# Performance work log

Hardware: AMD Instinct MI355X
Metric: run time of the kernel (lower is better)

Reference implementation:

```python
import jax, jax.numpy as jnp
import numpy as np

INDIM, OUTDIM, K, EXPAND = 256, 256, 3, 64
STRIDE, PAD, DIL, GROUPS = 1, 1, 1, 1


def _make_mask(rng):
    # expander connectivity: indim == outdim, so use the 'else' branch of the
    # torch code: for each input channel, pick EXPAND output channels.
    m = np.zeros((OUTDIM, INDIM), dtype=np.float32)
    for i in range(INDIM):
        x = rng.permutation(OUTDIM)[:EXPAND]
        m[x, i] = 1.0
    # repeat over the kernel spatial dims
    return np.broadcast_to(m[:, :, None, None], (OUTDIM, INDIM, K, K)).copy()


def setup_inputs() -> dict:
    key = jax.random.key(0)
    k1, k2 = jax.random.split(key)
    x = jax.random.normal(k1, (32, INDIM, 56, 56), dtype=jnp.float32)
    # kaiming_normal_(mode='fan_out'): std = sqrt(2 / (outdim * k * k))
    std = np.sqrt(2.0 / (OUTDIM * K * K)).astype(np.float32)
    weight = jax.random.normal(k2, (OUTDIM, INDIM, K, K), dtype=jnp.float32) * std
    mask = jnp.asarray(_make_mask(np.random.default_rng(0)))
    return {"x": x, "weight": weight, "mask": mask}


def reference(x, weight, mask) -> jnp.ndarray:
    w = weight * mask  # zero out non-expander connections
    return jax.lax.conv_general_dilated(
        x, w,
        window_strides=(STRIDE, STRIDE),
        padding=((PAD, PAD), (PAD, PAD)),
        rhs_dilation=(DIL, DIL),
        feature_group_count=GROUPS,
        dimension_numbers=("NCHW", "OIHW", "NCHW"),
    )
```

## Files before the change

kernel.cpp:

```cpp
#include <hip/hip_runtime.h>
#include <hip/hip_bf16.h>

typedef short short8 __attribute__((ext_vector_type(8)));
typedef float float4v __attribute__((ext_vector_type(4)));

#define NIMG 32
#define CIN 256
#define COUT 256
#define HH 56
#define WW 56
#define HP 58
#define WP 58
#define PIXIMG (HH * WW)
#define TOTPIX (NIMG * PIXIMG)
#define OUTSTRIDE_N (COUT * PIXIMG)
#define TR_BLOCKS (NIMG * HP * 4)

static constexpr size_t XT_ELEMS = (size_t)NIMG * HP * WP * CIN;
static constexpr size_t WT_ELEMS = (size_t)9 * COUT * CIN;

static __device__ __forceinline__ unsigned short f2bf(float f) {
    unsigned int u = __builtin_bit_cast(unsigned int, f);
    u = (u + 0x7fffu + ((u >> 16) & 1u)) >> 16;
    return (unsigned short)u;
}

static __device__ __forceinline__ void gl16(const unsigned short* g, char* l) {
    __builtin_amdgcn_global_load_lds(
        (const __attribute__((address_space(1))) void*)g,
        (__attribute__((address_space(3))) void*)l, 16, 0, 0);
}

__global__ __launch_bounds__(256) void k_pre(const float* __restrict__ x,
                                             const float* __restrict__ wgt,
                                             const float* __restrict__ msk,
                                             unsigned short* __restrict__ xt,
                                             unsigned short* __restrict__ wt) {
    int t = threadIdx.x;
    if (blockIdx.x >= TR_BLOCKS) {
        int g = (blockIdx.x - TR_BLOCKS) * 256 + t;
        const float* wp = wgt + (size_t)g * 9;
        const float* mp = msk + (size_t)g * 9;
#pragma unroll
        for (int tap = 0; tap < 9; ++tap)
            wt[(size_t)tap * (COUT * CIN) + g] = f2bf(wp[tap] * mp[tap]);
        return;
    }
    int b   = blockIdx.x;
    int icb = b & 3;
    int hp  = (b >> 2) % HP;
    int n   = b / (4 * HP);
    unsigned short* rowb = xt + ((size_t)(n * HP + hp) * WP) * CIN + icb * 64;

    if (hp == 0 || hp == HP - 1) {
        for (int idx = t; idx < WP * 8; idx += 256) {
            int wq = idx >> 3, q = idx & 7;
            *(uint4*)(rowb + (size_t)wq * CIN + q * 8) = (uint4){0, 0, 0, 0};
        }
        return;
    }
    int h = hp - 1;
    __shared__ __align__(16) char lds[64 * 128];
    int w = t & 63, icl0 = t >> 6;
    if (w < WW) {
        const float* src = x + ((size_t)(n * CIN + icb * 64 + icl0) * HH + h) * WW + w;
#pragma unroll
        for (int j = 0; j < 16; ++j) {
            float v = src[(size_t)(j * 4) * PIXIMG];
            int icl = icl0 + j * 4;
            *(unsigned short*)(lds + w * 128 + ((icl * 2) ^ ((w & 7) << 4))) = f2bf(v);
        }
    }
    __syncthreads();
    int ic4 = t & 15, wr = t >> 4;
    unsigned short* dst = rowb + (size_t)CIN + ic4 * 4;
#pragma unroll
    for (int p = 0; p < 4; ++p) {
        int w2 = wr + p * 16;
        if (w2 < WW) {
            uint2 v = *(const uint2*)(lds + w2 * 128 + ((ic4 * 8) ^ ((w2 & 7) << 4)));
            *(uint2*)(dst + (size_t)w2 * CIN) = v;
        }
    }
    if (t < 32) {
        int col = (t >> 4) * (WP - 1);
        *(uint2*)(rowb + (size_t)col * CIN + (t & 15) * 4) = (uint2){0, 0};
    }
}

__global__ __launch_bounds__(256, 4) void k_conv(const unsigned short* __restrict__ xt,
                                                 const unsigned short* __restrict__ wt,
                                                 float* __restrict__ out) {
    __shared__ __align__(16) char lds[64 * 132 * 4];

    const int t    = threadIdx.x;
    const int lane = t & 63;
    const int wid  = t >> 6;
    const int woc  = wid >> 1;
    const int wpx  = wid & 1;

    const int b0 = blockIdx.x;
    const int b  = (b0 & 7) * 196 + (b0 >> 3);
    const int ptile = b >> 1;
    const int ocb   = b & 1;

    const int rl  = lane >> 3;
    const int sc  = ((lane & 7) ^ rl) * 8;
    const unsigned short* aS[4];
    const unsigned short* bS[4];
    char* dA[4];
    char* dB[4];
#pragma unroll
    for (int c = 0; c < 4; ++c) {
        int r = wid * 32 + c * 8 + rl;
        aS[c] = wt + (size_t)(ocb * 128 + r) * CIN + sc;
        int pg  = ptile * 128 + r;
        int n   = pg / PIXIMG;
        int rem = pg - n * PIXIMG;
        int h   = rem / WW, w = rem - h * WW;
        bS[c] = xt + ((size_t)((n * HP + h) * WP + w)) * CIN + sc;
        dA[c] = lds + (wid * 32 + c * 8) * 128;
        dB[c] = lds + 16384 + (wid * 32 + c * 8) * 128;
    }

    const int l15  = lane & 15;
    const int lg   = lane >> 4;
    const int swzf = (lane & 7) << 4;
    int colk[2];
    colk[0] = (lg * 16) ^ swzf;
    colk[1] = (64 + lg * 16) ^ swzf;
    int rowA[4], rowB[4];
#pragma unroll
    for (int i = 0; i < 4; ++i) {
        rowA[i] = (woc * 64 + i * 16 + l15) * 128;
        rowB[i] = 16384 + (wpx * 64 + i * 16 + l15) * 128;
    }

    float4v acc[4][4];
#pragma unroll
    for (int i = 0; i < 4; ++i)
#pragma unroll
        for (int j = 0; j < 4; ++j)
            acc[i][j] = (float4v){0.f, 0.f, 0.f, 0.f};

#pragma unroll 1
    for (int s = 0; s < 36; ++s) {
        const int tap = s >> 2;
        const int dh  = (tap * 86) >> 8;
        const int dw  = tap - dh * 3;
        const size_t ao = (size_t)tap * (COUT * CIN) + (size_t)((s & 3) << 6);
        const size_t bo = (size_t)(dh * WP + dw) * CIN + (size_t)((s & 3) << 6);
#pragma unroll
        for (int c = 0; c < 4; ++c) gl16(aS[c] + ao, dA[c]);
#pragma unroll
        for (int c = 0; c < 4; ++c) gl16(bS[c] + bo, dB[c]);
        __syncthreads();
#pragma unroll
        for (int kk = 0; kk < 2; ++kk) {
            short8 af[4], bfr[4];
#pragma unroll
            for (int i = 0; i < 4; ++i)
                af[i] = *(const short8*)(lds + rowA[i] + colk[kk]);
#pragma unroll
            for (int i = 0; i < 4; ++i)
                bfr[i] = *(const short8*)(lds + rowB[i] + colk[kk]);
#pragma unroll
            for (int oi = 0; oi < 4; ++oi)
#pragma unroll
                for (int pi = 0; pi < 4; ++pi)
                    acc[oi][pi] = __builtin_amdgcn_mfma_f32_16x16x32_bf16(
                        af[oi], bfr[pi], acc[oi][pi], 0, 0, 0);
        }
        __syncthreads();
    }

    float* ep = (float*)lds;
#pragma unroll 1
    for (int c = 0; c < 2; ++c) {
        if (woc == c) {
#pragma unroll
            for (int oi = 0; oi < 4; ++oi)
#pragma unroll
                for (int pi = 0; pi < 4; ++pi)
#pragma unroll
                    for (int r = 0; r < 4; ++r)
                        ep[(oi * 16 + lg * 4 + r) * 132 +
                           (wpx * 64 + pi * 16 + l15)] = acc[oi][pi][r];
        }
        __syncthreads();
        const int rrow = t >> 5;
        const int rcol = (t & 31) * 4;
        int pg  = ptile * 128 + rcol;
        int n2  = pg / PIXIMG;
        int rem = pg - n2 * PIXIMG;
        float* ob = out + (size_t)n2 * OUTSTRIDE_N +
                    (size_t)(ocb * 128 + c * 64) * PIXIMG + rem;
#pragma unroll
        for (int rd = 0; rd < 8; ++rd) {
            int row = rd * 8 + rrow;
            float4v v = *(const float4v*)&ep[row * 132 + rcol];
            *(float4v*)(ob + (size_t)row * PIXIMG) = v;
        }
        __syncthreads();
    }
}

__global__ __launch_bounds__(256) void k_naive(const float* __restrict__ x,
                                               const float* __restrict__ wg,
                                               const float* __restrict__ mk,
                                               float* __restrict__ out, int total) {
    int idx = blockIdx.x * 256 + threadIdx.x;
    if (idx >= total) return;
    int w  = idx % WW;
    int h  = (idx / WW) % HH;
    int oc = (idx / PIXIMG) % COUT;
    int n  = idx / (COUT * PIXIMG);
    float s = 0.f;
    for (int ic = 0; ic < CIN; ++ic) {
        const float* xp = x + (size_t)(n * CIN + ic) * PIXIMG;
        const float* wp = wg + (size_t)(oc * CIN + ic) * 9;
        const float* mp = mk + (size_t)(oc * CIN + ic) * 9;
#pragma unroll
        for (int kh = 0; kh < 3; ++kh) {
            int hy = h + kh - 1;
            if ((unsigned)hy >= HH) continue;
#pragma unroll
            for (int kw = 0; kw < 3; ++kw) {
                int wx = w + kw - 1;
                if ((unsigned)wx >= WW) continue;
                s += xp[hy * WW + wx] * wp[kh * 3 + kw] * mp[kh * 3 + kw];
            }
        }
    }
    out[idx] = s;
}

extern "C" void kernel_launch(void* const* d_in, const int* in_sizes, int n_in,
                              void* d_out, int out_size, void* d_ws, size_t ws_size,
                              hipStream_t stream) {
    const float* x  = (const float*)d_in[0];
    const float* wg = (const float*)d_in[1];
    const float* mk = (const float*)d_in[2];
    float* out = (float*)d_out;

    size_t need = XT_ELEMS * 2 + WT_ELEMS * 2 + 256;
    if (ws_size < need) {
        int total = NIMG * COUT * PIXIMG;
        k_naive<<<(total + 255) / 256, 256, 0, stream>>>(x, wg, mk, out, total);
        return;
    }

    unsigned short* xt = (unsigned short*)d_ws;
    unsigned short* wt = (unsigned short*)((char*)d_ws + XT_ELEMS * 2);

    k_pre<<<TR_BLOCKS + (COUT * CIN) / 256, 256, 0, stream>>>(x, wg, mk, xt, wt);
    k_conv<<<(TOTPIX / 128) * 2, 256, 0, stream>>>(xt, wt, out);
}
```

Before: 151.4 us.

## Reuse a halo-extended input slab in LDS across all nine conv taps

The implicit-GEMM conv now tiles over padded pixel positions. Each block loads a 248-row input slab, covering its 128 pixels plus a one-row halo on each side, into LDS once per 64-channel block. All nine taps read from that slab at shifted row offsets, so the input is no longer reloaded for every tap. Output is written with per-element validity checks that drop padding positions, which wastes some compute and turns the epilogue into scalar stores. The larger LDS footprint lowers the occupancy target from 4 to 3 blocks per CU.

Result: slower. 155.8 us (+2.9%).

```diff
diff --git a/kernel.cpp b/kernel.cpp
--- a/kernel.cpp
+++ b/kernel.cpp
@@ -12,11 +12,13 @@
 #define HP 58
 #define WP 58
 #define PIXIMG (HH * WW)
-#define TOTPIX (NIMG * PIXIMG)
+#define QIMG (HP * WP)
+#define QTOT (NIMG * QIMG)
+#define NTILE (QTOT / 128)
 #define OUTSTRIDE_N (COUT * PIXIMG)
 #define TR_BLOCKS (NIMG * HP * 4)
 
-static constexpr size_t XT_ELEMS = (size_t)NIMG * HP * WP * CIN;
+static constexpr size_t XT_ELEMS = (size_t)QTOT * CIN;
 static constexpr size_t WT_ELEMS = (size_t)9 * COUT * CIN;
 
 static __device__ __forceinline__ unsigned short f2bf(float f) {
@@ -88,10 +90,10 @@
     }
 }
 
-__global__ __launch_bounds__(256, 4) void k_conv(const unsigned short* __restrict__ xt,
+__global__ __launch_bounds__(256, 3) void k_conv(const unsigned short* __restrict__ xt,
                                                  const unsigned short* __restrict__ wt,
                                                  float* __restrict__ out) {
-    __shared__ __align__(16) char lds[64 * 132 * 4];
+    __shared__ __align__(16) char lds[48128];
 
     const int t    = threadIdx.x;
     const int lane = t & 63;
@@ -99,28 +101,23 @@
     const int woc  = wid >> 1;
     const int wpx  = wid & 1;
 
-    const int b0 = blockIdx.x;
-    const int b  = (b0 & 7) * 196 + (b0 >> 3);
-    const int ptile = b >> 1;
-    const int ocb   = b & 1;
-
-    const int rl  = lane >> 3;
-    const int sc  = ((lane & 7) ^ rl) * 8;
+    const int xcd = blockIdx.x & 7;
+    const int idx = blockIdx.x >> 3;
+    const int wg  = (xcd < 2) ? xcd * 211 + idx : 422 + (xcd - 2) * 210 + idx;
+    const int ptile = wg >> 1;
+    const int ocb   = wg & 1;
+    const int q0    = ptile * 128;
+
+    const int rl = lane >> 3;
+    const int sc = ((lane & 7) ^ rl) * 8;
+
     const unsigned short* aS[4];
-    const unsigned short* bS[4];
     char* dA[4];
-    char* dB[4];
 #pragma unroll
     for (int c = 0; c < 4; ++c) {
         int r = wid * 32 + c * 8 + rl;
         aS[c] = wt + (size_t)(ocb * 128 + r) * CIN + sc;
-        int pg  = ptile * 128 + r;
-        int n   = pg / PIXIMG;
-        int rem = pg - n * PIXIMG;
-        int h   = rem / WW, w = rem - h * WW;
-        bS[c] = xt + ((size_t)((n * HP + h) * WP + w)) * CIN + sc;
         dA[c] = lds + (wid * 32 + c * 8) * 128;
-        dB[c] = lds + 16384 + (wid * 32 + c * 8) * 128;
     }
 
     const int l15  = lane & 15;
@@ -129,12 +126,10 @@
     int colk[2];
     colk[0] = (lg * 16) ^ swzf;
     colk[1] = (64 + lg * 16) ^ swzf;
-    int rowA[4], rowB[4];
-#pragma unroll
-    for (int i = 0; i < 4; ++i) {
+    int rowA[4];
+#pragma unroll
+    for (int i = 0; i < 4; ++i)
         rowA[i] = (woc * 64 + i * 16 + l15) * 128;
-        rowB[i] = 16384 + (wpx * 64 + i * 16 + l15) * 128;
-    }
 
     float4v acc[4][4];
 #pragma unroll
@@ -144,37 +139,62 @@
             acc[i][j] = (float4v){0.f, 0.f, 0.f, 0.f};
 
 #pragma unroll 1
-    for (int s = 0; s < 36; ++s) {
-        const int tap = s >> 2;
-        const int dh  = (tap * 86) >> 8;
-        const int dw  = tap - dh * 3;
-        const size_t ao = (size_t)tap * (COUT * CIN) + (size_t)((s & 3) << 6);
-        const size_t bo = (size_t)(dh * WP + dw) * CIN + (size_t)((s & 3) << 6);
-#pragma unroll
-        for (int c = 0; c < 4; ++c) gl16(aS[c] + ao, dA[c]);
-#pragma unroll
-        for (int c = 0; c < 4; ++c) gl16(bS[c] + bo, dB[c]);
-        __syncthreads();
-#pragma unroll
-        for (int kk = 0; kk < 2; ++kk) {
-            short8 af[4], bfr[4];
-#pragma unroll
-            for (int i = 0; i < 4; ++i)
-                af[i] = *(const short8*)(lds + rowA[i] + colk[kk]);
-#pragma unroll
-            for (int i = 0; i < 4; ++i)
-                bfr[i] = *(const short8*)(lds + rowB[i] + colk[kk]);
-#pragma unroll
-            for (int oi = 0; oi < 4; ++oi)
-#pragma unroll
-                for (int pi = 0; pi < 4; ++pi)
-                    acc[oi][pi] = __builtin_amdgcn_mfma_f32_16x16x32_bf16(
-                        af[oi], bfr[pi], acc[oi][pi], 0, 0, 0);
-        }
-        __syncthreads();
+    for (int icb = 0; icb < 4; ++icb) {
+        for (int k = wid; k < 31; k += 4) {
+            int qr = q0 - 59 + 8 * k;
+            qr = (qr < 0) ? 0 : ((qr > QTOT - 8) ? QTOT - 8 : qr);
+            gl16(xt + (size_t)(qr + rl) * CIN + icb * 64 + sc,
+                 lds + 16384 + k * 1024);
+        }
+#pragma unroll
+        for (int tap = 0; tap < 9; ++tap) {
+            const size_t ao = (size_t)tap * (COUT * CIN) + icb * 64;
+#pragma unroll
+            for (int c = 0; c < 4; ++c) gl16(aS[c] + ao, dA[c]);
+            __syncthreads();
+            const int dh    = (tap * 86) >> 8;
+            const int dw    = tap - dh * 3;
+            const int delta = (dh - 1) * WP + (dw - 1);
+            const int rbb   = 59 + delta + wpx * 64 + l15;
+#pragma unroll
+            for (int kk = 0; kk < 2; ++kk) {
+                short8 af[4], bf[4];
+#pragma unroll
+                for (int i = 0; i < 4; ++i)
+                    af[i] = *(const short8*)(lds + rowA[i] + colk[kk]);
+#pragma unroll
+                for (int i = 0; i < 4; ++i) {
+                    int rb = rbb + i * 16;
+                    bf[i] = *(const short8*)(lds + 16384 + rb * 128 +
+                                             ((kk * 64 + lg * 16) ^ ((rb & 7) << 4)));
+                }
+#pragma unroll
+                for (int oi = 0; oi < 4; ++oi)
+#pragma unroll
+                    for (int pi = 0; pi < 4; ++pi)
+                        acc[oi][pi] = __builtin_amdgcn_mfma_f32_16x16x32_bf16(
+                            af[oi], bf[pi], acc[oi][pi], 0, 0, 0);
+            }
+            __syncthreads();
+        }
     }
 
     float* ep = (float*)lds;
+    const int rcol = (t & 31) * 4;
+    bool vld[4];
+    float* obase[4];
+#pragma unroll
+    for (int cc = 0; cc < 4; ++cc) {
+        int q  = q0 + rcol + cc;
+        int n  = q / QIMG;
+        int r2 = q - n * QIMG;
+        int hp = r2 / WP;
+        int wp = r2 - hp * WP;
+        vld[cc] = ((unsigned)(hp - 1) < (unsigned)HH) &&
+                  ((unsigned)(wp - 1) < (unsigned)WW);
+        obase[cc] = out + (size_t)n * OUTSTRIDE_N +
+                    (size_t)(ocb * 128) * PIXIMG + (hp - 1) * WW + (wp - 1);
+    }
 #pragma unroll 1
     for (int c = 0; c < 2; ++c) {
         if (woc == c) {
@@ -189,17 +209,14 @@
         }
         __syncthreads();
         const int rrow = t >> 5;
-        const int rcol = (t & 31) * 4;
-        int pg  = ptile * 128 + rcol;
-        int n2  = pg / PIXIMG;
-        int rem = pg - n2 * PIXIMG;
-        float* ob = out + (size_t)n2 * OUTSTRIDE_N +
-                    (size_t)(ocb * 128 + c * 64) * PIXIMG + rem;
 #pragma unroll
         for (int rd = 0; rd < 8; ++rd) {
             int row = rd * 8 + rrow;
             float4v v = *(const float4v*)&ep[row * 132 + rcol];
-            *(float4v*)(ob + (size_t)row * PIXIMG) = v;
+            size_t ro = (size_t)(c * 64 + row) * PIXIMG;
+#pragma unroll
+            for (int cc = 0; cc < 4; ++cc)
+                if (vld[cc]) obase[cc][ro] = v[cc];
         }
         __syncthreads();
     }
@@ -254,5 +271,5 @@
     unsigned short* wt = (unsigned short*)((char*)d_ws + XT_ELEMS * 2);
 
     k_pre<<<TR_BLOCKS + (COUT * CIN) / 256, 256, 0, stream>>>(x, wg, mk, xt, wt);
-    k_conv<<<(TOTPIX / 128) * 2, 256, 0, stream>>>(xt, wt, out);
-}
+    k_conv<<<NTILE * 2, 256, 0, stream>>>(xt, wt, out);
+}
```

## Pre-swizzle weights into MFMA fragment layout and load A directly to registers

Applied to the files above, without the earlier changes.

The weight preprocessing now writes bf16 weights in a fragment-ordered layout, so each lane can load its MFMA A operand straight from global memory as a contiguous short8. The conv kernel no longer stages weights through LDS; only the input tile goes through LDS, which halves LDS traffic and the LDS reads per step. It also lowers the occupancy hint from 4 to 3 waves to leave room for the extra registers holding both k-halves of A. The cost is more global/L2 load traffic from every wave, with latency that is only partly hidden before the barrier.

Result: slower. 160.3 us (+5.9%).

```diff
diff --git a/kernel.cpp b/kernel.cpp
--- a/kernel.cpp
+++ b/kernel.cpp
@@ -35,15 +35,20 @@
                                              const float* __restrict__ wgt,
                                              const float* __restrict__ msk,
                                              unsigned short* __restrict__ xt,
-                                             unsigned short* __restrict__ wt) {
+                                             unsigned short* __restrict__ wtF) {
     int t = threadIdx.x;
     if (blockIdx.x >= TR_BLOCKS) {
-        int g = (blockIdx.x - TR_BLOCKS) * 256 + t;
+        int g  = (blockIdx.x - TR_BLOCKS) * 256 + t;
+        int oc = g >> 8;
+        int ic = g & 255;
+        int fbl = ((ic >> 6) << 3) + (((ic >> 5) & 1) << 2) + ((ic >> 3) & 3);
+        int j   = ic & 7;
         const float* wp = wgt + (size_t)g * 9;
         const float* mp = msk + (size_t)g * 9;
 #pragma unroll
         for (int tap = 0; tap < 9; ++tap)
-            wt[(size_t)tap * (COUT * CIN) + g] = f2bf(wp[tap] * mp[tap]);
+            wtF[(size_t)(tap * 32 + fbl) * 2048 + oc * 8 + j] =
+                f2bf(wp[tap] * mp[tap]);
         return;
     }
     int b   = blockIdx.x;
@@ -88,8 +93,8 @@
     }
 }
 
-__global__ __launch_bounds__(256, 4) void k_conv(const unsigned short* __restrict__ xt,
-                                                 const unsigned short* __restrict__ wt,
+__global__ __launch_bounds__(256, 3) void k_conv(const unsigned short* __restrict__ xt,
+                                                 const unsigned short* __restrict__ wtF,
                                                  float* __restrict__ out) {
     __shared__ __align__(16) char lds[64 * 132 * 4];
 
@@ -106,21 +111,17 @@
 
     const int rl  = lane >> 3;
     const int sc  = ((lane & 7) ^ rl) * 8;
-    const unsigned short* aS[4];
     const unsigned short* bS[4];
-    char* dA[4];
     char* dB[4];
 #pragma unroll
     for (int c = 0; c < 4; ++c) {
         int r = wid * 32 + c * 8 + rl;
-        aS[c] = wt + (size_t)(ocb * 128 + r) * CIN + sc;
         int pg  = ptile * 128 + r;
         int n   = pg / PIXIMG;
         int rem = pg - n * PIXIMG;
         int h   = rem / WW, w = rem - h * WW;
         bS[c] = xt + ((size_t)((n * HP + h) * WP + w)) * CIN + sc;
-        dA[c] = lds + (wid * 32 + c * 8) * 128;
-        dB[c] = lds + 16384 + (wid * 32 + c * 8) * 128;
+        dB[c] = lds + (wid * 32 + c * 8) * 128;
     }
 
     const int l15  = lane & 15;
@@ -129,12 +130,13 @@
     int colk[2];
     colk[0] = (lg * 16) ^ swzf;
     colk[1] = (64 + lg * 16) ^ swzf;
-    int rowA[4], rowB[4];
-#pragma unroll
-    for (int i = 0; i < 4; ++i) {
-        rowA[i] = (woc * 64 + i * 16 + l15) * 128;
-        rowB[i] = 16384 + (wpx * 64 + i * 16 + l15) * 128;
-    }
+    int rowB[4];
+#pragma unroll
+    for (int i = 0; i < 4; ++i)
+        rowB[i] = (wpx * 64 + i * 16 + l15) * 128;
+
+    const unsigned short* aBase =
+        wtF + (size_t)lg * 2048 + (size_t)(ocb * 128 + woc * 64 + l15) * 8;
 
     float4v acc[4][4];
 #pragma unroll
@@ -148,19 +150,22 @@
         const int tap = s >> 2;
         const int dh  = (tap * 86) >> 8;
         const int dw  = tap - dh * 3;
-        const size_t ao = (size_t)tap * (COUT * CIN) + (size_t)((s & 3) << 6);
         const size_t bo = (size_t)(dh * WP + dw) * CIN + (size_t)((s & 3) << 6);
-#pragma unroll
-        for (int c = 0; c < 4; ++c) gl16(aS[c] + ao, dA[c]);
+        const unsigned short* aStep = aBase + (size_t)s * 16384;
+
+        short8 af0[4], af1[4];
 #pragma unroll
         for (int c = 0; c < 4; ++c) gl16(bS[c] + bo, dB[c]);
+#pragma unroll
+        for (int i = 0; i < 4; ++i)
+            af0[i] = *(const short8*)(aStep + i * 128);
+#pragma unroll
+        for (int i = 0; i < 4; ++i)
+            af1[i] = *(const short8*)(aStep + 8192 + i * 128);
         __syncthreads();
 #pragma unroll
         for (int kk = 0; kk < 2; ++kk) {
-            short8 af[4], bfr[4];
-#pragma unroll
-            for (int i = 0; i < 4; ++i)
-                af[i] = *(const short8*)(lds + rowA[i] + colk[kk]);
+            short8 bfr[4];
 #pragma unroll
             for (int i = 0; i < 4; ++i)
                 bfr[i] = *(const short8*)(lds + rowB[i] + colk[kk]);
@@ -169,7 +174,7 @@
 #pragma unroll
                 for (int pi = 0; pi < 4; ++pi)
                     acc[oi][pi] = __builtin_amdgcn_mfma_f32_16x16x32_bf16(
-                        af[oi], bfr[pi], acc[oi][pi], 0, 0, 0);
+                        kk ? af1[oi] : af0[oi], bfr[pi], acc[oi][pi], 0, 0, 0);
         }
         __syncthreads();
     }
@@ -250,9 +255,9 @@
         return;
     }
 
-    unsigned short* xt = (unsigned short*)d_ws;
-    unsigned short* wt = (unsigned short*)((char*)d_ws + XT_ELEMS * 2);
-
-    k_pre<<<TR_BLOCKS + (COUT * CIN) / 256, 256, 0, stream>>>(x, wg, mk, xt, wt);
-    k_conv<<<(TOTPIX / 128) * 2, 256, 0, stream>>>(xt, wt, out);
-}
+    unsigned short* xt  = (unsigned short*)d_ws;
+    unsigned short* wtF = (unsigned short*)((char*)d_ws + XT_ELEMS * 2);
+
+    k_pre<<<TR_BLOCKS + (COUT * CIN) / 256, 256, 0, stream>>>(x, wg, mk, xt, wtF);
+    k_conv<<<(TOTPIX / 128) * 2, 256, 0, stream>>>(xt, wtF, out);
+}
```

## Halve conv block pixel tile to 64 with two waves per block

Applied to the files above, without the earlier changes.

The implicit-GEMM conv block shrinks from 128 output channels × 128 pixels on four waves to 128 channels × 64 pixels on two waves. Each wave now owns a full 64-channel slice and loads its own weight rows, and the LDS footprint and epilogue staging shrink to match. The grid doubles and the launch bounds change to 128 threads, aiming for more resident blocks and better latency hiding. The cost is lower data reuse: weight tiles are fetched twice as often per unit of compute, which raises L2 and LDS-fill traffic.

New measurement: 168.4 us. 11.3% more time.

```diff
diff --git a/kernel.cpp b/kernel.cpp
--- a/kernel.cpp
+++ b/kernel.cpp
@@ -25,7 +25,7 @@
     return (unsigned short)u;
 }
 
-static __device__ __forceinline__ void gl16(const unsigned short* g, char* l) {
+static __device__ __forceinline__ void gl16(const unsigned short* g, const char* l) {
     __builtin_amdgcn_global_load_lds(
         (const __attribute__((address_space(1))) void*)g,
         (__attribute__((address_space(3))) void*)l, 16, 0, 0);
@@ -88,40 +88,35 @@
     }
 }
 
-__global__ __launch_bounds__(256, 4) void k_conv(const unsigned short* __restrict__ xt,
+__global__ __launch_bounds__(128, 3) void k_conv(const unsigned short* __restrict__ xt,
                                                  const unsigned short* __restrict__ wt,
                                                  float* __restrict__ out) {
-    __shared__ __align__(16) char lds[64 * 132 * 4];
+    __shared__ __align__(16) char lds[24576];
 
     const int t    = threadIdx.x;
     const int lane = t & 63;
     const int wid  = t >> 6;
-    const int woc  = wid >> 1;
-    const int wpx  = wid & 1;
 
     const int b0 = blockIdx.x;
-    const int b  = (b0 & 7) * 196 + (b0 >> 3);
+    const int b  = (b0 & 7) * 392 + (b0 >> 3);
     const int ptile = b >> 1;
     const int ocb   = b & 1;
 
-    const int rl  = lane >> 3;
-    const int sc  = ((lane & 7) ^ rl) * 8;
-    const unsigned short* aS[4];
+    const int rl = lane >> 3;
+    const int sc = ((lane & 7) ^ rl) * 8;
+    const unsigned short* aSrc = wt + (size_t)(ocb * 128 + wid * 64 + rl) * CIN + sc;
+    char* const ldsA = lds + (wid * 64) * 128;
     const unsigned short* bS[4];
-    char* dA[4];
-    char* dB[4];
 #pragma unroll
     for (int c = 0; c < 4; ++c) {
-        int r = wid * 32 + c * 8 + rl;
-        aS[c] = wt + (size_t)(ocb * 128 + r) * CIN + sc;
-        int pg  = ptile * 128 + r;
+        int r   = wid * 32 + c * 8 + rl;
+        int pg  = ptile * 64 + r;
         int n   = pg / PIXIMG;
         int rem = pg - n * PIXIMG;
         int h   = rem / WW, w = rem - h * WW;
         bS[c] = xt + ((size_t)((n * HP + h) * WP + w)) * CIN + sc;
-        dA[c] = lds + (wid * 32 + c * 8) * 128;
-        dB[c] = lds + 16384 + (wid * 32 + c * 8) * 128;
-    }
+    }
+    char* const ldsB = lds + 16384 + (wid * 32) * 128;
 
     const int l15  = lane & 15;
     const int lg   = lane >> 4;
@@ -132,8 +127,8 @@
     int rowA[4], rowB[4];
 #pragma unroll
     for (int i = 0; i < 4; ++i) {
-        rowA[i] = (woc * 64 + i * 16 + l15) * 128;
-        rowB[i] = 16384 + (wpx * 64 + i * 16 + l15) * 128;
+        rowA[i] = (wid * 64 + i * 16 + l15) * 128;
+        rowB[i] = 16384 + (i * 16 + l15) * 128;
     }
 
     float4v acc[4][4];
@@ -151,9 +146,9 @@
         const size_t ao = (size_t)tap * (COUT * CIN) + (size_t)((s & 3) << 6);
         const size_t bo = (size_t)(dh * WP + dw) * CIN + (size_t)((s & 3) << 6);
 #pragma unroll
-        for (int c = 0; c < 4; ++c) gl16(aS[c] + ao, dA[c]);
-#pragma unroll
-        for (int c = 0; c < 4; ++c) gl16(bS[c] + bo, dB[c]);
+        for (int c = 0; c < 8; ++c) gl16(aSrc + ao + c * (8 * CIN), ldsA + c * 1024);
+#pragma unroll
+        for (int c = 0; c < 4; ++c) gl16(bS[c] + bo, ldsB + c * 1024);
         __syncthreads();
 #pragma unroll
         for (int kk = 0; kk < 2; ++kk) {
@@ -177,28 +172,28 @@
     float* ep = (float*)lds;
 #pragma unroll 1
     for (int c = 0; c < 2; ++c) {
-        if (woc == c) {
+        if (wid == c) {
 #pragma unroll
             for (int oi = 0; oi < 4; ++oi)
 #pragma unroll
                 for (int pi = 0; pi < 4; ++pi)
 #pragma unroll
                     for (int r = 0; r < 4; ++r)
-                        ep[(oi * 16 + lg * 4 + r) * 132 +
-                           (wpx * 64 + pi * 16 + l15)] = acc[oi][pi][r];
-        }
-        __syncthreads();
-        const int rrow = t >> 5;
-        const int rcol = (t & 31) * 4;
-        int pg  = ptile * 128 + rcol;
+                        ep[(oi * 16 + lg * 4 + r) * 68 + (pi * 16 + l15)] =
+                            acc[oi][pi][r];
+        }
+        __syncthreads();
+        const int erow = t >> 4;
+        const int ecol = (t & 15) * 4;
+        int pg  = ptile * 64 + ecol;
         int n2  = pg / PIXIMG;
         int rem = pg - n2 * PIXIMG;
         float* ob = out + (size_t)n2 * OUTSTRIDE_N +
                     (size_t)(ocb * 128 + c * 64) * PIXIMG + rem;
 #pragma unroll
-        for (int rd = 0; rd < 8; ++rd) {
-            int row = rd * 8 + rrow;
-            float4v v = *(const float4v*)&ep[row * 132 + rcol];
+        for (int p = 0; p < 8; ++p) {
+            int row = p * 8 + erow;
+            float4v v = *(const float4v*)&ep[row * 68 + ecol];
             *(float4v*)(ob + (size_t)row * PIXIMG) = v;
         }
         __syncthreads();
@@ -254,5 +249,5 @@
     unsigned short* wt = (unsigned short*)((char*)d_ws + XT_ELEMS * 2);
 
     k_pre<<<TR_BLOCKS + (COUT * CIN) / 256, 256, 0, stream>>>(x, wg, mk, xt, wt);
-    k_conv<<<(TOTPIX / 128) * 2, 256, 0, stream>>>(xt, wt, out);
-}
+    k_conv<<<(TOTPIX / 64) * 2, 128, 0, stream>>>(xt, wt, out);
+}
```
